# Kernel optimization log

Measured on AMD Instinct MI355X. Metric: run time of the kernel, lower is better.

## Reference

```python
import jax, jax.numpy as jnp
import numpy as np

_BIG = 1e4  # kornia uses 1e4 as the 'infinity' for masked-out kernel positions


def _windows(img, pad_val):
    """Return the 9 shifted 3x3 neighborhoods of img, stacked on axis 0.
    img: [B,C,H,W] -> [9,B,C,H,W]. Border padded with pad_val so padded
    pixels never win the min (erosion) / max (dilation), matching kornia.
    """
    B, C, H, W = img.shape
    p = jnp.pad(img, ((0, 0), (0, 0), (1, 1), (1, 1)), constant_values=pad_val)
    return jnp.stack([p[..., i:i + H, j:j + W]
                      for i in range(3) for j in range(3)], axis=0)


def _erosion(img, mask):
    w = _windows(img, _BIG)
    return jnp.min(jnp.where(mask, w, _BIG), axis=0)


def _dilation(img, mask):
    w = _windows(img, -_BIG)
    return jnp.max(jnp.where(mask, w, -_BIG), axis=0)


def setup_inputs() -> dict:
    key = jax.random.key(0)
    img = jax.random.uniform(key, (8, 3, 1024, 1024), dtype=jnp.float32)
    # kernel0: symmetric 3x3 cross structuring element
    kernel = jnp.array([[0, 1, 0], [1, 1, 1], [0, 1, 0]], dtype=jnp.int32)
    return {"img": img, "kernel": kernel}


def reference(img, kernel):
    # morphological opening = erosion followed by dilation, same structuring element
    mask = (kernel.reshape(9, 1, 1, 1, 1) == 1)
    eroded = _erosion(img, mask)
    opened = _dilation(eroded, mask)
    return opened
```

## Files before the change

kernel.cpp:

```cpp
#include <hip/hip_runtime.h>

#define BIGV 1e4f

constexpr int RH = 8;
constexpr int TY = 2;

struct Raw { float4 M; float2 X; };
struct Row { float2 L; float4 M; float2 R; };
struct Ero { float eL; float4 eM; float eR; };

__device__ __forceinline__ float min3f(float a, float b, float c) { return fminf(fminf(a, b), c); }
__device__ __forceinline__ float max3f(float a, float b, float c) { return fmaxf(fmaxf(a, b), c); }

__device__ __forceinline__ Raw load_raw(const float* __restrict__ img, int y, int gx,
                                        int lx, int H, int W) {
    Raw r;
    r.X = make_float2(BIGV, BIGV);
    if (y >= 0 && y < H) {
        const float* q = img + (size_t)y * W;
        r.M = *(const float4*)(q + gx);
        if (lx == 0  && gx > 0)     r.X = *(const float2*)(q + gx - 2);
        if (lx == 63 && gx + 4 < W) r.X = *(const float2*)(q + gx + 4);
    } else {
        r.M = make_float4(BIGV, BIGV, BIGV, BIGV);
    }
    return r;
}

__device__ __forceinline__ Row rowify(const Raw& r, int lx) {
    Row o;
    o.M = r.M;
    float lz = __shfl_up(r.M.z, 1, 64);
    float lw = __shfl_up(r.M.w, 1, 64);
    float rx = __shfl_down(r.M.x, 1, 64);
    float ry = __shfl_down(r.M.y, 1, 64);
    o.L = (lx == 0)  ? r.X : make_float2(lz, lw);
    o.R = (lx == 63) ? r.X : make_float2(rx, ry);
    return o;
}

__device__ __forceinline__ float rget(const Row& r, int q) {
    switch (q) {
        case -2: return r.L.x; case -1: return r.L.y;
        case 0:  return r.M.x; case 1:  return r.M.y;
        case 2:  return r.M.z; case 3:  return r.M.w;
        case 4:  return r.R.x; default: return r.R.y;
    }
}
__device__ __forceinline__ float eget(const Ero& e, int q) {
    switch (q) {
        case -1: return e.eL;
        case 0:  return e.eM.x; case 1:  return e.eM.y;
        case 2:  return e.eM.z; case 3:  return e.eM.w;
        default: return e.eR;
    }
}

__device__ __forceinline__ Ero erode_cross(const Row& a, const Row& b, const Row& c,
                                           int r, int H, int gx, int W) {
    Ero e;
    if (r >= 0 && r < H) {
        e.eL   = min3f(min3f(a.L.y, b.L.y, c.L.y), b.L.x, b.M.x);
        e.eM.x = min3f(min3f(a.M.x, b.M.x, c.M.x), b.L.y, b.M.y);
        e.eM.y = min3f(min3f(a.M.y, b.M.y, c.M.y), b.M.x, b.M.z);
        e.eM.z = min3f(min3f(a.M.z, b.M.z, c.M.z), b.M.y, b.M.w);
        e.eM.w = min3f(min3f(a.M.w, b.M.w, c.M.w), b.M.z, b.R.x);
        e.eR   = min3f(min3f(a.R.x, b.R.x, c.R.x), b.M.w, b.R.y);
        if (gx == 0)     e.eL = -BIGV;
        if (gx + 4 >= W) e.eR = -BIGV;
    } else {
        e.eL = -BIGV; e.eM = make_float4(-BIGV, -BIGV, -BIGV, -BIGV); e.eR = -BIGV;
    }
    return e;
}

__device__ __forceinline__ float4 dilate_cross(const Ero& t, const Ero& m, const Ero& b) {
    float4 o;
    o.x = max3f(max3f(t.eM.x, m.eM.x, b.eM.x), m.eL,   m.eM.y);
    o.y = max3f(max3f(t.eM.y, m.eM.y, b.eM.y), m.eM.x, m.eM.z);
    o.z = max3f(max3f(t.eM.z, m.eM.z, b.eM.z), m.eM.y, m.eM.w);
    o.w = max3f(max3f(t.eM.w, m.eM.w, b.eM.w), m.eM.z, m.eR);
    return o;
}

__device__ __forceinline__ Ero erode_gen(const Row& a, const Row& b, const Row& c,
                                         const bool* m, int r, int H, int gx, int W) {
    Ero e;
    if (r >= 0 && r < H) {
        float v[6];
#pragma unroll
        for (int p = 0; p < 6; ++p) {
            float acc = BIGV;
#pragma unroll
            for (int k = 0; k < 9; ++k) {
                const int di = k / 3, dj = k % 3;
                const Row& rr = (di == 0) ? a : ((di == 1) ? b : c);
                float t = rget(rr, p - 2 + dj);
                acc = fminf(acc, m[k] ? t : BIGV);
            }
            v[p] = acc;
        }
        e.eL = v[0]; e.eM.x = v[1]; e.eM.y = v[2]; e.eM.z = v[3]; e.eM.w = v[4]; e.eR = v[5];
        if (gx == 0)     e.eL = -BIGV;
        if (gx + 4 >= W) e.eR = -BIGV;
    } else {
        e.eL = -BIGV; e.eM = make_float4(-BIGV, -BIGV, -BIGV, -BIGV); e.eR = -BIGV;
    }
    return e;
}

__device__ __forceinline__ float4 dilate_gen(const Ero& e0, const Ero& e1, const Ero& e2,
                                             const bool* m) {
    float o[4];
#pragma unroll
    for (int j = 0; j < 4; ++j) {
        float acc = -BIGV;
#pragma unroll
        for (int k = 0; k < 9; ++k) {
            const int di = k / 3, dj = k % 3;
            const Ero& ee = (di == 0) ? e0 : ((di == 1) ? e1 : e2);
            float t = eget(ee, j + dj - 1);
            acc = fmaxf(acc, m[k] ? t : -BIGV);
        }
        o[j] = acc;
    }
    return make_float4(o[0], o[1], o[2], o[3]);
}

template <bool CROSS>
__device__ __forceinline__ void run(const float* __restrict__ img, float* __restrict__ out,
                                    const bool* m, int gx, int y0, int lx, int H, int W) {
    Raw rb = load_raw(img, y0 - 2, gx, lx, H, W);
    Raw rc = load_raw(img, y0 - 1, gx, lx, H, W);
    Raw rd = load_raw(img, y0,     gx, lx, H, W);
    Raw re = load_raw(img, y0 + 1, gx, lx, H, W);
    Raw p2 = load_raw(img, y0 + 2, gx, lx, H, W);
    Raw p3 = load_raw(img, y0 + 3, gx, lx, H, W);

    Row B   = rowify(rb, lx);
    Row C   = rowify(rc, lx);
    Row Cur = rowify(rd, lx);
    Ero E0 = CROSS ? erode_cross(B, C, Cur, y0 - 1, H, gx, W)
                   : erode_gen(B, C, Cur, m, y0 - 1, H, gx, W);
    Row Nxt = rowify(re, lx);
    Ero E1 = CROSS ? erode_cross(C, Cur, Nxt, y0, H, gx, W)
                   : erode_gen(C, Cur, Nxt, m, y0, H, gx, W);

#pragma unroll
    for (int i = 0; i < RH; ++i) {
        const int y = y0 + i;
        Raw pn = p3;
        if (i < RH - 2)
            pn = load_raw(img, y + 4, gx, lx, H, W);
        Row N = rowify(p2, lx);
        Ero E2 = CROSS ? erode_cross(Cur, Nxt, N, y + 1, H, gx, W)
                       : erode_gen(Cur, Nxt, N, m, y + 1, H, gx, W);
        float4 o = CROSS ? dilate_cross(E0, E1, E2) : dilate_gen(E0, E1, E2, m);
        *(float4*)(out + (size_t)y * W + gx) = o;
        Cur = Nxt; Nxt = N;
        E0 = E1; E1 = E2;
        p2 = p3; p3 = pn;
    }
}

__global__ __launch_bounds__(128) void opening_kernel(
    const float* __restrict__ img, const int* __restrict__ kern,
    float* __restrict__ out, int H, int W)
{
    const int lx = threadIdx.x & 63;
    const int ty = threadIdx.x >> 6;
    const int gx = blockIdx.x * 256 + lx * 4;
    const int y0 = (blockIdx.y * TY + ty) * RH;
    const size_t pbase = (size_t)blockIdx.z * H * W;

    bool m[9];
#pragma unroll
    for (int k = 0; k < 9; ++k) m[k] = (kern[k] == 1);

    const bool cross = m[1] && m[3] && m[4] && m[5] && m[7] &&
                       !m[0] && !m[2] && !m[6] && !m[8];

    if (cross) run<true >(img + pbase, out + pbase, m, gx, y0, lx, H, W);
    else       run<false>(img + pbase, out + pbase, m, gx, y0, lx, H, W);
}

extern "C" void kernel_launch(void* const* d_in, const int* in_sizes, int n_in,
                              void* d_out, int out_size, void* d_ws, size_t ws_size,
                              hipStream_t stream) {
    const float* img  = (const float*)d_in[0];
    const int*   kern = (const int*)d_in[1];
    float*       out  = (float*)d_out;

    const int H = 1024, W = 1024;
    const int planes = in_sizes[0] / (H * W);

    dim3 block(128);
    dim3 grid(W / 256, H / (TY * RH), planes);
    opening_kernel<<<grid, block, 0, stream>>>(img, kern, out, H, W);
}
```

Measured before the change: 179.6 us.

## Process full image rows per wavefront with 16 pixels per lane

Each 64-lane wavefront now spans the full 1024-pixel row, with each lane owning 16 contiguous pixels loaded as four float4s. This removes the cross-block horizontal halo loads, replaces image-border handling with lane-edge constants, and cuts shuffle overhead per pixel. In exchange, register use grows, the grid has four times fewer blocks, the row prefetch depth drops to one, and an occupancy hint is added to launch bounds.

```diff
diff --git a/kernel.cpp b/kernel.cpp
--- a/kernel.cpp
+++ b/kernel.cpp
@@ -2,176 +2,152 @@
 
 #define BIGV 1e4f
 
-constexpr int RH = 8;
-constexpr int TY = 2;
+constexpr int RH  = 8;
+constexpr int TY  = 2;
+constexpr int PXL = 16;
 
-struct Raw { float4 M; float2 X; };
-struct Row { float2 L; float4 M; float2 R; };
-struct Ero { float eL; float4 eM; float eR; };
+struct Raw { float4 v[4]; };
+struct Row { float l0, l1; float m[PXL]; float r0, r1; };
+struct Ero { float e[PXL + 2]; };
 
-__device__ __forceinline__ float min3f(float a, float b, float c) { return fminf(fminf(a, b), c); }
-__device__ __forceinline__ float max3f(float a, float b, float c) { return fmaxf(fmaxf(a, b), c); }
-
-__device__ __forceinline__ Raw load_raw(const float* __restrict__ img, int y, int gx,
+__device__ __forceinline__ Raw load_raw(const float* __restrict__ img, int y,
                                         int lx, int H, int W) {
     Raw r;
-    r.X = make_float2(BIGV, BIGV);
     if (y >= 0 && y < H) {
-        const float* q = img + (size_t)y * W;
-        r.M = *(const float4*)(q + gx);
-        if (lx == 0  && gx > 0)     r.X = *(const float2*)(q + gx - 2);
-        if (lx == 63 && gx + 4 < W) r.X = *(const float2*)(q + gx + 4);
+        const float4* q = (const float4*)(img + (size_t)y * W + lx * PXL);
+        r.v[0] = q[0]; r.v[1] = q[1]; r.v[2] = q[2]; r.v[3] = q[3];
     } else {
-        r.M = make_float4(BIGV, BIGV, BIGV, BIGV);
+#pragma unroll
+        for (int i = 0; i < 4; ++i) r.v[i] = make_float4(BIGV, BIGV, BIGV, BIGV);
     }
     return r;
 }
 
 __device__ __forceinline__ Row rowify(const Raw& r, int lx) {
     Row o;
-    o.M = r.M;
-    float lz = __shfl_up(r.M.z, 1, 64);
-    float lw = __shfl_up(r.M.w, 1, 64);
-    float rx = __shfl_down(r.M.x, 1, 64);
-    float ry = __shfl_down(r.M.y, 1, 64);
-    o.L = (lx == 0)  ? r.X : make_float2(lz, lw);
-    o.R = (lx == 63) ? r.X : make_float2(rx, ry);
+#pragma unroll
+    for (int i = 0; i < 4; ++i) {
+        o.m[4*i+0] = r.v[i].x; o.m[4*i+1] = r.v[i].y;
+        o.m[4*i+2] = r.v[i].z; o.m[4*i+3] = r.v[i].w;
+    }
+    float lz = __shfl_up(r.v[3].z, 1, 64);
+    float lw = __shfl_up(r.v[3].w, 1, 64);
+    float rx = __shfl_down(r.v[0].x, 1, 64);
+    float ry = __shfl_down(r.v[0].y, 1, 64);
+    o.l0 = (lx == 0)  ? BIGV : lz;
+    o.l1 = (lx == 0)  ? BIGV : lw;
+    o.r0 = (lx == 63) ? BIGV : rx;
+    o.r1 = (lx == 63) ? BIGV : ry;
     return o;
 }
 
 __device__ __forceinline__ float rget(const Row& r, int q) {
-    switch (q) {
-        case -2: return r.L.x; case -1: return r.L.y;
-        case 0:  return r.M.x; case 1:  return r.M.y;
-        case 2:  return r.M.z; case 3:  return r.M.w;
-        case 4:  return r.R.x; default: return r.R.y;
-    }
-}
-__device__ __forceinline__ float eget(const Ero& e, int q) {
-    switch (q) {
-        case -1: return e.eL;
-        case 0:  return e.eM.x; case 1:  return e.eM.y;
-        case 2:  return e.eM.z; case 3:  return e.eM.w;
-        default: return e.eR;
-    }
+    if (q == -2)      return r.l0;
+    if (q == -1)      return r.l1;
+    if (q == PXL)     return r.r0;
+    if (q == PXL + 1) return r.r1;
+    return r.m[q];
 }
 
-__device__ __forceinline__ Ero erode_cross(const Row& a, const Row& b, const Row& c,
-                                           int r, int H, int gx, int W) {
+template <bool CROSS>
+__device__ __forceinline__ Ero erode(const Row& a, const Row& b, const Row& c,
+                                     const bool* m, int r, int H, int lx) {
     Ero e;
     if (r >= 0 && r < H) {
-        e.eL   = min3f(min3f(a.L.y, b.L.y, c.L.y), b.L.x, b.M.x);
-        e.eM.x = min3f(min3f(a.M.x, b.M.x, c.M.x), b.L.y, b.M.y);
-        e.eM.y = min3f(min3f(a.M.y, b.M.y, c.M.y), b.M.x, b.M.z);
-        e.eM.z = min3f(min3f(a.M.z, b.M.z, c.M.z), b.M.y, b.M.w);
-        e.eM.w = min3f(min3f(a.M.w, b.M.w, c.M.w), b.M.z, b.R.x);
-        e.eR   = min3f(min3f(a.R.x, b.R.x, c.R.x), b.M.w, b.R.y);
-        if (gx == 0)     e.eL = -BIGV;
-        if (gx + 4 >= W) e.eR = -BIGV;
+#pragma unroll
+        for (int p = 0; p < PXL + 2; ++p) {
+            float acc;
+            if (CROSS) {
+                acc = fminf(fminf(rget(a, p-1), rget(c, p-1)),
+                            fminf(fminf(rget(b, p-2), rget(b, p)), rget(b, p-1)));
+            } else {
+                acc = BIGV;
+#pragma unroll
+                for (int k = 0; k < 9; ++k) {
+                    const int di = k / 3, dj = k % 3;
+                    const Row& rr = (di == 0) ? a : ((di == 1) ? b : c);
+                    float t = rget(rr, p - 2 + dj);
+                    acc = fminf(acc, m[k] ? t : BIGV);
+                }
+            }
+            e.e[p] = acc;
+        }
+        if (lx == 0)  e.e[0]       = -BIGV;
+        if (lx == 63) e.e[PXL + 1] = -BIGV;
     } else {
-        e.eL = -BIGV; e.eM = make_float4(-BIGV, -BIGV, -BIGV, -BIGV); e.eR = -BIGV;
+#pragma unroll
+        for (int p = 0; p < PXL + 2; ++p) e.e[p] = -BIGV;
     }
     return e;
 }
 
-__device__ __forceinline__ float4 dilate_cross(const Ero& t, const Ero& m, const Ero& b) {
-    float4 o;
-    o.x = max3f(max3f(t.eM.x, m.eM.x, b.eM.x), m.eL,   m.eM.y);
-    o.y = max3f(max3f(t.eM.y, m.eM.y, b.eM.y), m.eM.x, m.eM.z);
-    o.z = max3f(max3f(t.eM.z, m.eM.z, b.eM.z), m.eM.y, m.eM.w);
-    o.w = max3f(max3f(t.eM.w, m.eM.w, b.eM.w), m.eM.z, m.eR);
-    return o;
-}
-
-__device__ __forceinline__ Ero erode_gen(const Row& a, const Row& b, const Row& c,
-                                         const bool* m, int r, int H, int gx, int W) {
-    Ero e;
-    if (r >= 0 && r < H) {
-        float v[6];
+template <bool CROSS>
+__device__ __forceinline__ void dilate(const Ero& t, const Ero& mi, const Ero& bo,
+                                       const bool* m, float* o ) {
 #pragma unroll
-        for (int p = 0; p < 6; ++p) {
-            float acc = BIGV;
+    for (int j = 0; j < PXL; ++j) {
+        float acc;
+        if (CROSS) {
+            acc = fmaxf(fmaxf(t.e[j+1], bo.e[j+1]),
+                        fmaxf(fmaxf(mi.e[j], mi.e[j+2]), mi.e[j+1]));
+        } else {
+            acc = -BIGV;
 #pragma unroll
             for (int k = 0; k < 9; ++k) {
                 const int di = k / 3, dj = k % 3;
-                const Row& rr = (di == 0) ? a : ((di == 1) ? b : c);
-                float t = rget(rr, p - 2 + dj);
-                acc = fminf(acc, m[k] ? t : BIGV);
+                const Ero& ee = (di == 0) ? t : ((di == 1) ? mi : bo);
+                acc = fmaxf(acc, m[k] ? ee.e[j + dj] : -BIGV);
             }
-            v[p] = acc;
-        }
-        e.eL = v[0]; e.eM.x = v[1]; e.eM.y = v[2]; e.eM.z = v[3]; e.eM.w = v[4]; e.eR = v[5];
-        if (gx == 0)     e.eL = -BIGV;
-        if (gx + 4 >= W) e.eR = -BIGV;
-    } else {
-        e.eL = -BIGV; e.eM = make_float4(-BIGV, -BIGV, -BIGV, -BIGV); e.eR = -BIGV;
-    }
-    return e;
-}
-
-__device__ __forceinline__ float4 dilate_gen(const Ero& e0, const Ero& e1, const Ero& e2,
-                                             const bool* m) {
-    float o[4];
-#pragma unroll
-    for (int j = 0; j < 4; ++j) {
-        float acc = -BIGV;
-#pragma unroll
-        for (int k = 0; k < 9; ++k) {
-            const int di = k / 3, dj = k % 3;
-            const Ero& ee = (di == 0) ? e0 : ((di == 1) ? e1 : e2);
-            float t = eget(ee, j + dj - 1);
-            acc = fmaxf(acc, m[k] ? t : -BIGV);
         }
         o[j] = acc;
     }
-    return make_float4(o[0], o[1], o[2], o[3]);
 }
 
 template <bool CROSS>
-__device__ __forceinline__ void run(const float* __restrict__ img, float* __restrict__ out,
-                                    const bool* m, int gx, int y0, int lx, int H, int W) {
-    Raw rb = load_raw(img, y0 - 2, gx, lx, H, W);
-    Raw rc = load_raw(img, y0 - 1, gx, lx, H, W);
-    Raw rd = load_raw(img, y0,     gx, lx, H, W);
-    Raw re = load_raw(img, y0 + 1, gx, lx, H, W);
-    Raw p2 = load_raw(img, y0 + 2, gx, lx, H, W);
-    Raw p3 = load_raw(img, y0 + 3, gx, lx, H, W);
+__device__ __forceinline__ void run(const float* __restrict__ img,
+                                    float* __restrict__ out, const bool* m,
+                                    int y0, int lx, int H, int W) {
+    Raw rb = load_raw(img, y0 - 2, lx, H, W);
+    Raw rc = load_raw(img, y0 - 1, lx, H, W);
+    Raw rd = load_raw(img, y0,     lx, H, W);
+    Raw re = load_raw(img, y0 + 1, lx, H, W);
+    Raw p  = load_raw(img, y0 + 2, lx, H, W);
 
     Row B   = rowify(rb, lx);
     Row C   = rowify(rc, lx);
     Row Cur = rowify(rd, lx);
-    Ero E0 = CROSS ? erode_cross(B, C, Cur, y0 - 1, H, gx, W)
-                   : erode_gen(B, C, Cur, m, y0 - 1, H, gx, W);
+    Ero E0 = erode<CROSS>(B, C, Cur, m, y0 - 1, H, lx);
     Row Nxt = rowify(re, lx);
-    Ero E1 = CROSS ? erode_cross(C, Cur, Nxt, y0, H, gx, W)
-                   : erode_gen(C, Cur, Nxt, m, y0, H, gx, W);
+    Ero E1 = erode<CROSS>(C, Cur, Nxt, m, y0, H, lx);
 
 #pragma unroll
     for (int i = 0; i < RH; ++i) {
         const int y = y0 + i;
-        Raw pn = p3;
-        if (i < RH - 2)
-            pn = load_raw(img, y + 4, gx, lx, H, W);
-        Row N = rowify(p2, lx);
-        Ero E2 = CROSS ? erode_cross(Cur, Nxt, N, y + 1, H, gx, W)
-                       : erode_gen(Cur, Nxt, N, m, y + 1, H, gx, W);
-        float4 o = CROSS ? dilate_cross(E0, E1, E2) : dilate_gen(E0, E1, E2, m);
-        *(float4*)(out + (size_t)y * W + gx) = o;
+        Raw pn = p;
+        if (i < RH - 1)
+            pn = load_raw(img, y + 3, lx, H, W);
+        Row N = rowify(p, lx);
+        Ero E2 = erode<CROSS>(Cur, Nxt, N, m, y + 1, H, lx);
+        float o[PXL];
+        dilate<CROSS>(E0, E1, E2, m, o);
+        float4* qo = (float4*)(out + (size_t)y * W + lx * PXL);
+#pragma unroll
+        for (int t4 = 0; t4 < 4; ++t4)
+            qo[t4] = make_float4(o[4*t4], o[4*t4+1], o[4*t4+2], o[4*t4+3]);
         Cur = Nxt; Nxt = N;
         E0 = E1; E1 = E2;
-        p2 = p3; p3 = pn;
+        p = pn;
     }
 }
 
-__global__ __launch_bounds__(128) void opening_kernel(
+__global__ __launch_bounds__(128, 3) void opening_kernel(
     const float* __restrict__ img, const int* __restrict__ kern,
     float* __restrict__ out, int H, int W)
 {
     const int lx = threadIdx.x & 63;
     const int ty = threadIdx.x >> 6;
-    const int gx = blockIdx.x * 256 + lx * 4;
-    const int y0 = (blockIdx.y * TY + ty) * RH;
-    const size_t pbase = (size_t)blockIdx.z * H * W;
+    const int y0 = (blockIdx.x * TY + ty) * RH;
+    const size_t pbase = (size_t)blockIdx.y * H * W;
 
     bool m[9];
 #pragma unroll
@@ -180,8 +156,8 @@
     const bool cross = m[1] && m[3] && m[4] && m[5] && m[7] &&
                        !m[0] && !m[2] && !m[6] && !m[8];
 
-    if (cross) run<true >(img + pbase, out + pbase, m, gx, y0, lx, H, W);
-    else       run<false>(img + pbase, out + pbase, m, gx, y0, lx, H, W);
+    if (cross) run<true >(img + pbase, out + pbase, m, y0, lx, H, W);
+    else       run<false>(img + pbase, out + pbase, m, y0, lx, H, W);
 }
 
 extern "C" void kernel_launch(void* const* d_in, const int* in_sizes, int n_in,
@@ -195,6 +171,6 @@
     const int planes = in_sizes[0] / (H * W);
 
     dim3 block(128);
-    dim3 grid(W / 256, H / (TY * RH), planes);
+    dim3 grid(H / (TY * RH), planes);
     opening_kernel<<<grid, block, 0, stream>>>(img, kern, out, H, W);
 }
```

Result: slower. 190.2 us (+5.9%).

## Stream full rows into LDS via async global_load_lds ring buffer

Applied to the files above, without the earlier changes.

Each 64-thread block now owns a full 1024-wide row strip of 8 rows and streams input rows into a 5-slot LDS ring using global_load_lds DMA, with explicit vmcnt waits to overlap loads with compute. Horizontal neighbours are read from LDS instead of lane shuffles plus extra edge loads. The grid is flattened with a block-index swizzle across planes. This trades per-thread register pressure and hand-tuned waitcnt accounting (fragile if the compiler reorders memory ops) for fewer redundant halo loads and deeper prefetch.

```diff
diff --git a/kernel.cpp b/kernel.cpp
--- a/kernel.cpp
+++ b/kernel.cpp
@@ -1,42 +1,60 @@
 #include <hip/hip_runtime.h>
+#include <stdint.h>
 
 #define BIGV 1e4f
 
-constexpr int RH = 8;
-constexpr int TY = 2;
-
-struct Raw { float4 M; float2 X; };
+constexpr int RH    = 8;
+constexpr int NSLOT = 5;
+constexpr int WROW  = 1024;
+
 struct Row { float2 L; float4 M; float2 R; };
 struct Ero { float eL; float4 eM; float eR; };
 
+#define WAITVM(n)  asm volatile("s_waitcnt vmcnt(" #n ")" ::: "memory")
+#define WAITALL0() asm volatile("s_waitcnt vmcnt(0) lgkmcnt(0)" ::: "memory")
+#define WAITLG0()  asm volatile("s_waitcnt lgkmcnt(0)" ::: "memory")
+#define SCHED0()   __builtin_amdgcn_sched_barrier(0)
+
 __device__ __forceinline__ float min3f(float a, float b, float c) { return fminf(fminf(a, b), c); }
 __device__ __forceinline__ float max3f(float a, float b, float c) { return fmaxf(fmaxf(a, b), c); }
 
-__device__ __forceinline__ Raw load_raw(const float* __restrict__ img, int y, int gx,
-                                        int lx, int H, int W) {
-    Raw r;
-    r.X = make_float2(BIGV, BIGV);
-    if (y >= 0 && y < H) {
-        const float* q = img + (size_t)y * W;
-        r.M = *(const float4*)(q + gx);
-        if (lx == 0  && gx > 0)     r.X = *(const float2*)(q + gx - 2);
-        if (lx == 63 && gx + 4 < W) r.X = *(const float2*)(q + gx + 4);
+__device__ __forceinline__ void gld16(const void* g, void* l) {
+    __builtin_amdgcn_global_load_lds(
+        (const __attribute__((address_space(1))) void*)g,
+        (__attribute__((address_space(3))) void*)l, 16, 0, 0);
+}
+
+__device__ __forceinline__ void dma_row(const float* __restrict__ img, float* lds,
+                                        int slot, int r, int H, int W, int lx) {
+    const int rc = min(max(r, 0), H - 1);
+    const float* src = img + (size_t)rc * W + 4 * lx;
+    float* dst = lds + slot * WROW;
+#pragma unroll
+    for (int c = 0; c < 4; ++c)
+        gld16(src + c * 256, dst + c * 256);
+}
+
+__device__ __forceinline__ void read_row4(const float* lds, int slot, int lx,
+                                          int r, int H, Row* w) {
+    if (r >= 0 && r < H) {
+        const float* sb = lds + slot * WROW;
+#pragma unroll
+        for (int c = 0; c < 4; ++c) {
+            const int fb = c * 256 + 4 * lx;
+            w[c].M = *(const float4*)(sb + fb);
+            if (c == 0 && lx == 0) w[c].L = make_float2(BIGV, BIGV);
+            else                   w[c].L = *(const float2*)(sb + fb - 2);
+            if (c == 3 && lx == 63) w[c].R = make_float2(BIGV, BIGV);
+            else                    w[c].R = *(const float2*)(sb + fb + 4);
+        }
     } else {
-        r.M = make_float4(BIGV, BIGV, BIGV, BIGV);
-    }
-    return r;
-}
-
-__device__ __forceinline__ Row rowify(const Raw& r, int lx) {
-    Row o;
-    o.M = r.M;
-    float lz = __shfl_up(r.M.z, 1, 64);
-    float lw = __shfl_up(r.M.w, 1, 64);
-    float rx = __shfl_down(r.M.x, 1, 64);
-    float ry = __shfl_down(r.M.y, 1, 64);
-    o.L = (lx == 0)  ? r.X : make_float2(lz, lw);
-    o.R = (lx == 63) ? r.X : make_float2(rx, ry);
-    return o;
+#pragma unroll
+        for (int c = 0; c < 4; ++c) {
+            w[c].L = make_float2(BIGV, BIGV);
+            w[c].M = make_float4(BIGV, BIGV, BIGV, BIGV);
+            w[c].R = make_float2(BIGV, BIGV);
+        }
+    }
 }
 
 __device__ __forceinline__ float rget(const Row& r, int q) {
@@ -119,8 +137,7 @@
         for (int k = 0; k < 9; ++k) {
             const int di = k / 3, dj = k % 3;
             const Ero& ee = (di == 0) ? e0 : ((di == 1) ? e1 : e2);
-            float t = eget(ee, j + dj - 1);
-            acc = fmaxf(acc, m[k] ? t : -BIGV);
+            acc = fmaxf(acc, m[k] ? eget(ee, j + dj - 1) : -BIGV);
         }
         o[j] = acc;
     }
@@ -129,59 +146,90 @@
 
 template <bool CROSS>
 __device__ __forceinline__ void run(const float* __restrict__ img, float* __restrict__ out,
-                                    const bool* m, int gx, int y0, int lx, int H, int W) {
-    Raw rb = load_raw(img, y0 - 2, gx, lx, H, W);
-    Raw rc = load_raw(img, y0 - 1, gx, lx, H, W);
-    Raw rd = load_raw(img, y0,     gx, lx, H, W);
-    Raw re = load_raw(img, y0 + 1, gx, lx, H, W);
-    Raw p2 = load_raw(img, y0 + 2, gx, lx, H, W);
-    Raw p3 = load_raw(img, y0 + 3, gx, lx, H, W);
-
-    Row B   = rowify(rb, lx);
-    Row C   = rowify(rc, lx);
-    Row Cur = rowify(rd, lx);
-    Ero E0 = CROSS ? erode_cross(B, C, Cur, y0 - 1, H, gx, W)
-                   : erode_gen(B, C, Cur, m, y0 - 1, H, gx, W);
-    Row Nxt = rowify(re, lx);
-    Ero E1 = CROSS ? erode_cross(C, Cur, Nxt, y0, H, gx, W)
-                   : erode_gen(C, Cur, Nxt, m, y0, H, gx, W);
+                                    float* lds, const bool* m, int y0, int lx, int H, int W) {
+    WAITALL0();
+#pragma unroll
+    for (int k = 0; k < NSLOT; ++k) dma_row(img, lds, k, y0 - 2 + k, H, W, lx);
+    SCHED0();
+    WAITVM(4);
+    SCHED0();
+    Row B[4], C[4], Cur[4], Nxt[4];
+    read_row4(lds, 0, lx, y0 - 2, H, B);
+    read_row4(lds, 1, lx, y0 - 1, H, C);
+    read_row4(lds, 2, lx, y0,     H, Cur);
+    read_row4(lds, 3, lx, y0 + 1, H, Nxt);
+    WAITLG0();
+    SCHED0();
+    dma_row(img, lds, 0, y0 + 3, H, W, lx);
+    dma_row(img, lds, 1, y0 + 4, H, W, lx);
+    dma_row(img, lds, 2, y0 + 5, H, W, lx);
+    SCHED0();
+    Ero E0[4], E1[4];
+#pragma unroll
+    for (int c = 0; c < 4; ++c) {
+        const int gx = c * 256 + 4 * lx;
+        E0[c] = CROSS ? erode_cross(B[c], C[c], Cur[c], y0 - 1, H, gx, W)
+                      : erode_gen (B[c], C[c], Cur[c], m, y0 - 1, H, gx, W);
+        E1[c] = CROSS ? erode_cross(C[c], Cur[c], Nxt[c], y0, H, gx, W)
+                      : erode_gen (C[c], Cur[c], Nxt[c], m, y0, H, gx, W);
+    }
 
 #pragma unroll
     for (int i = 0; i < RH; ++i) {
         const int y = y0 + i;
-        Raw pn = p3;
-        if (i < RH - 2)
-            pn = load_raw(img, y + 4, gx, lx, H, W);
-        Row N = rowify(p2, lx);
-        Ero E2 = CROSS ? erode_cross(Cur, Nxt, N, y + 1, H, gx, W)
-                       : erode_gen(Cur, Nxt, N, m, y + 1, H, gx, W);
-        float4 o = CROSS ? dilate_cross(E0, E1, E2) : dilate_gen(E0, E1, E2, m);
-        *(float4*)(out + (size_t)y * W + gx) = o;
-        Cur = Nxt; Nxt = N;
-        E0 = E1; E1 = E2;
-        p2 = p3; p3 = pn;
-    }
-}
-
-__global__ __launch_bounds__(128) void opening_kernel(
+        if      (i == 0) WAITVM(12);
+        else if (i == 1) WAITVM(16);
+        else if (i == 2) WAITVM(20);
+        else if (i == 3) WAITVM(24);
+        else if (i == 4) WAITVM(24);
+        else if (i == 5) WAITVM(20);
+        else if (i == 6) WAITVM(16);
+        else             WAITVM(12);
+        SCHED0();
+        Row N[4];
+        read_row4(lds, (i + 4) % NSLOT, lx, y + 2, H, N);
+#pragma unroll
+        for (int c = 0; c < 4; ++c) {
+            const int gx = c * 256 + 4 * lx;
+            Ero E2 = CROSS ? erode_cross(Cur[c], Nxt[c], N[c], y + 1, H, gx, W)
+                           : erode_gen (Cur[c], Nxt[c], N[c], m, y + 1, H, gx, W);
+            float4 o = CROSS ? dilate_cross(E0[c], E1[c], E2)
+                             : dilate_gen (E0[c], E1[c], E2, m);
+            *(float4*)(out + (size_t)y * W + gx) = o;
+            E0[c] = E1[c]; E1[c] = E2;
+            Cur[c] = Nxt[c]; Nxt[c] = N[c];
+        }
+        SCHED0();
+        if (i < RH - 4) {
+            dma_row(img, lds, (i + 3) % NSLOT, y + 6, H, W, lx);
+            SCHED0();
+        }
+    }
+}
+
+__global__ __launch_bounds__(64, 2) void opening_kernel(
     const float* __restrict__ img, const int* __restrict__ kern,
     float* __restrict__ out, int H, int W)
 {
-    const int lx = threadIdx.x & 63;
-    const int ty = threadIdx.x >> 6;
-    const int gx = blockIdx.x * 256 + lx * 4;
-    const int y0 = (blockIdx.y * TY + ty) * RH;
-    const size_t pbase = (size_t)blockIdx.z * H * W;
+    __shared__ float lds[NSLOT * WROW];
+    const int lx = threadIdx.x;
+
+    const int bid   = blockIdx.x;
+    const int chunk = gridDim.x >> 3;
+    const int swz   = (bid & 7) * chunk + (bid >> 3);
+    const int sy    = swz & 127;
+    const int plane = swz >> 7;
+    const int y0    = sy * RH;
+    const size_t pbase = (size_t)plane * H * W;
 
     bool m[9];
 #pragma unroll
     for (int k = 0; k < 9; ++k) m[k] = (kern[k] == 1);
-
     const bool cross = m[1] && m[3] && m[4] && m[5] && m[7] &&
                        !m[0] && !m[2] && !m[6] && !m[8];
 
-    if (cross) run<true >(img + pbase, out + pbase, m, gx, y0, lx, H, W);
-    else       run<false>(img + pbase, out + pbase, m, gx, y0, lx, H, W);
+    if (cross) run<true >(img + pbase, out + pbase, lds, m, y0, lx, H, W);
+    else       run<false>(img + pbase, out + pbase, lds, m, y0, lx, H, W);
 }
 
 extern "C" void kernel_launch(void* const* d_in, const int* in_sizes, int n_in,
@@ -194,7 +242,7 @@
     const int H = 1024, W = 1024;
     const int planes = in_sizes[0] / (H * W);
 
-    dim3 block(128);
-    dim3 grid(W / 256, H / (TY * RH), planes);
+    dim3 block(64);
+    dim3 grid((H / RH) * planes);
     opening_kernel<<<grid, block, 0, stream>>>(img, kern, out, H, W);
 }
```

Result: slower. 184.6 us (+2.8%).
